# Optimization experiments

Hardware: AMD Instinct MI355X
Metric: run time of the kernel (lower is better)

Reference implementation:

```python
import jax, jax.numpy as jnp
import numpy as np

def setup_inputs() -> dict:
    key = jax.random.key(0)
    k1, k2 = jax.random.split(key)
    B, S, D, R = 16, 1024, 1024, 128
    batch = jax.random.normal(k1, (B, S, D), dtype=jnp.float32)
    # probe parameter initialized uniform(-0.05, 0.05) as in the torch module
    proj = jax.random.uniform(k2, (D, R), dtype=jnp.float32, minval=-0.05, maxval=0.05)
    return {"batch": batch, "proj": proj}

def reference(batch, proj):
    # transformed: [B, S, R]
    t = jnp.matmul(batch, proj)
    # squared L2 distances for all pairs: ||t_i||^2 + ||t_j||^2 - 2 t_i . t_j
    sq_norms = jnp.sum(t * t, axis=-1)                      # [B, S]
    cross = jnp.einsum('bir,bjr->bij', t, t)                # [B, S, S]
    d = sq_norms[:, :, None] + sq_norms[:, None, :] - 2.0 * cross
    return jnp.maximum(d, 0.0)  # clamp tiny negative values from the identity
```

## Files before the change

kernel.cpp:

```cpp
#include <hip/hip_runtime.h>

typedef __attribute__((ext_vector_type(8))) __bf16 bf16x8;
typedef __attribute__((ext_vector_type(4))) float f32x4;
typedef const __attribute__((address_space(1))) unsigned int gu32;
typedef __attribute__((address_space(3))) unsigned int lu32;

#define B_ 16
#define S_ 1024
#define D_ 1024
#define R_ 128

__device__ __forceinline__ void gl16(const void* g, void* l) {
    __builtin_amdgcn_global_load_lds((gu32*)g, (lu32*)l, 16, 0, 0);
}

__global__ __launch_bounds__(256) void k_transpose(const float* __restrict__ proj,
                                                   __bf16* __restrict__ projT) {
    __shared__ __bf16 tile[64][66];
    const int k0 = blockIdx.x * 64;
    const int r0 = blockIdx.y * 64;
#pragma unroll
    for (int it = 0; it < 16; ++it) {
        int idx = it * 256 + threadIdx.x;
        int kk = idx >> 6, rr = idx & 63;
        tile[kk][rr] = (__bf16)proj[(size_t)(k0 + kk) * R_ + (r0 + rr)];
    }
    __syncthreads();
#pragma unroll
    for (int it = 0; it < 16; ++it) {
        int idx = it * 256 + threadIdx.x;
        int rr = idx >> 6, kk = idx & 63;
        projT[(size_t)(r0 + rr) * D_ + (k0 + kk)] = tile[kk][rr];
    }
}

__global__ __launch_bounds__(256, 4) void k_proj(const float* __restrict__ batch,
                                                 const __bf16* __restrict__ projT,
                                                 __bf16* __restrict__ t,
                                                 float* __restrict__ sqn) {
    __shared__ __align__(16) char smem[40960];
    const int wave = threadIdx.x >> 6;
    const int lane = threadIdx.x & 63;
    const int ln = lane & 15, q = lane >> 4;
    const int m0 = blockIdx.x * 16;

    const int arow = wave * 4 + (lane >> 4);
    const int aswz = ((arow & 7) << 5) | ((arow & 8) << 1);
    const char* ag = (const char*)batch + (size_t)(m0 + arow) * 4096
                   + (((lane & 15) * 16) ^ aswz);
    const int brx = wave * 8 + (lane >> 3);
    const int bswz = (brx & 7) << 4;
    const char* bg = (const char*)projT + (size_t)brx * 2048
                   + (((lane & 7) * 16) ^ bswz);
    char* const abuf0 = smem + wave * 1024;
    char* const bbuf0 = smem + 8192 + wave * 1024;

    const int raswz = ((ln & 7) << 5) | ((ln & 8) << 1);
    const int rbswz = (ln & 7) << 4;
    const int kq = q * 32;
    const int kq2 = q * 16;

    f32x4 acc[2];
    acc[0] = f32x4{0.f, 0.f, 0.f, 0.f};
    acc[1] = f32x4{0.f, 0.f, 0.f, 0.f};

    gl16(ag, abuf0);
#pragma unroll
    for (int s = 0; s < 4; ++s) gl16(bg + (size_t)s * 65536, bbuf0 + s * 4096);
    __syncthreads();

#pragma unroll 2
    for (int c = 0; c < 16; ++c) {
        const int cur = c & 1, nxt = cur ^ 1;
        if (c < 15) {
            gl16(ag + (c + 1) * 256, abuf0 + nxt * 4096);
#pragma unroll
            for (int s = 0; s < 4; ++s)
                gl16(bg + (size_t)s * 65536 + (c + 1) * 128,
                     bbuf0 + nxt * 16384 + s * 4096);
        }
        const char* ab = smem + cur * 4096 + ln * 256;
        const char* bb = smem + 8192 + cur * 16384 + ln * 128;
#pragma unroll
        for (int ks = 0; ks < 2; ++ks) {
            float4 lo = *(const float4*)(ab + ((ks * 128 + kq) ^ raswz));
            float4 hi = *(const float4*)(ab + ((ks * 128 + kq + 16) ^ raswz));
            bf16x8 af;
            af[0] = (__bf16)lo.x; af[1] = (__bf16)lo.y;
            af[2] = (__bf16)lo.z; af[3] = (__bf16)lo.w;
            af[4] = (__bf16)hi.x; af[5] = (__bf16)hi.y;
            af[6] = (__bf16)hi.z; af[7] = (__bf16)hi.w;
            const int ko = (ks * 64 + kq2) ^ rbswz;
            bf16x8 bf0 = *(const bf16x8*)(bb + (wave * 2 + 0) * 2048 + ko);
            bf16x8 bf1 = *(const bf16x8*)(bb + (wave * 2 + 1) * 2048 + ko);
            acc[0] = __builtin_amdgcn_mfma_f32_16x16x32_bf16(af, bf0, acc[0], 0, 0, 0);
            acc[1] = __builtin_amdgcn_mfma_f32_16x16x32_bf16(af, bf1, acc[1], 0, 0, 0);
        }
        __syncthreads();
    }

    float* sqpart = (float*)smem;
    float sq[4] = {0.f, 0.f, 0.f, 0.f};
#pragma unroll
    for (int p = 0; p < 2; ++p) {
        const int ni = wave * 2 + p;
        f32x4 v = acc[p];
#pragma unroll
        for (int r = 0; r < 4; ++r) {
            __bf16 h = (__bf16)v[r];
            t[(size_t)(m0 + q * 4 + r) * R_ + ni * 16 + ln] = h;
            float f = (float)h;
            sq[r] += f * f;
        }
    }
#pragma unroll
    for (int r = 0; r < 4; ++r) {
#pragma unroll
        for (int off = 1; off < 16; off <<= 1)
            sq[r] += __shfl_xor(sq[r], off, 64);
    }
    if (ln == 0) {
#pragma unroll
        for (int r = 0; r < 4; ++r) sqpart[wave * 16 + q * 4 + r] = sq[r];
    }
    __syncthreads();
    if (threadIdx.x < 16) {
        float s = sqpart[threadIdx.x] + sqpart[16 + threadIdx.x] +
                  sqpart[32 + threadIdx.x] + sqpart[48 + threadIdx.x];
        sqn[m0 + threadIdx.x] = s;
    }
}

__global__ __launch_bounds__(256, 2) void k_gram(const __bf16* __restrict__ t,
                                                 const float* __restrict__ sqn,
                                                 float* __restrict__ out) {
    __shared__ __align__(16) char smem[65536];
    const int b = blockIdx.z;
    const int wave = threadIdx.x >> 6, lane = threadIdx.x & 63;
    const int ln = lane & 15, q = lane >> 4;
    const int wi = wave >> 1, wj = wave & 1;
    const int i0b = blockIdx.y * 128, j0b = blockIdx.x * 128;
    const __bf16* tb = t + (size_t)b * S_ * R_;
    const float* sqb = sqn + (size_t)b * S_;

    const int grow = wave * 4 + (lane >> 4);
    const int gwin = ((lane & 15) * 16) ^ ((grow & 7) << 4);
    const char* agt = (const char*)tb + (size_t)(i0b + grow) * 256 + gwin;
    const char* bgt = (const char*)tb + (size_t)(j0b + grow) * 256 + gwin;
    char* const adst = smem + wave * 1024;
    char* const bdst = smem + 32768 + wave * 1024;
#pragma unroll
    for (int s = 0; s < 8; ++s) gl16(agt + (size_t)s * 4096, adst + s * 4096);
#pragma unroll
    for (int s = 0; s < 8; ++s) gl16(bgt + (size_t)s * 4096, bdst + s * 4096);

    float sqj[4];
#pragma unroll
    for (int ni = 0; ni < 4; ++ni) sqj[ni] = sqb[j0b + wj * 64 + ni * 16 + ln];
    __syncthreads();

    f32x4 acc[4][4];
#pragma unroll
    for (int mi = 0; mi < 4; ++mi)
#pragma unroll
        for (int ni = 0; ni < 4; ++ni) acc[mi][ni] = f32x4{0.f, 0.f, 0.f, 0.f};

    const int rsw = (ln & 7) << 4;
    const char* abA = smem + (size_t)(wi * 64 + ln) * 256;
    const char* abB = smem + 32768 + (size_t)(wj * 64 + ln) * 256;
#pragma unroll
    for (int ks = 0; ks < 4; ++ks) {
        const int ko = (ks * 64 + q * 16) ^ rsw;
        bf16x8 af[4], bfm[4];
#pragma unroll
        for (int mi = 0; mi < 4; ++mi)
            af[mi] = *(const bf16x8*)(abA + mi * 4096 + ko);
#pragma unroll
        for (int ni = 0; ni < 4; ++ni)
            bfm[ni] = *(const bf16x8*)(abB + ni * 4096 + ko);
#pragma unroll
        for (int mi = 0; mi < 4; ++mi)
#pragma unroll
            for (int ni = 0; ni < 4; ++ni)
                acc[mi][ni] = __builtin_amdgcn_mfma_f32_16x16x32_bf16(
                    af[mi], bfm[ni], acc[mi][ni], 0, 0, 0);
    }

    const int i0 = i0b + wi * 64, j0 = j0b + wj * 64;
    float* outb = out + (size_t)b * S_ * S_;
#pragma unroll
    for (int mi = 0; mi < 4; ++mi) {
#pragma unroll
        for (int r = 0; r < 4; ++r) {
            const int i = i0 + mi * 16 + q * 4 + r;
            const float si = sqb[i];
            float* orow = outb + (size_t)i * S_ + j0;
#pragma unroll
            for (int ni = 0; ni < 4; ++ni) {
                float v = si + sqj[ni] - 2.f * acc[mi][ni][r];
                orow[ni * 16 + ln] = fmaxf(v, 0.f);
            }
        }
    }
}

extern "C" void kernel_launch(void* const* d_in, const int* in_sizes, int n_in,
                              void* d_out, int out_size, void* d_ws, size_t ws_size,
                              hipStream_t stream) {
    const float* batch = (const float*)d_in[0];
    const float* proj  = (const float*)d_in[1];
    float* out = (float*)d_out;

    char* ws = (char*)d_ws;
    __bf16* t     = (__bf16*)ws;
    __bf16* projT = (__bf16*)(ws + (size_t)B_ * S_ * R_ * 2);
    float*  sqn   = (float*)(ws + (size_t)B_ * S_ * R_ * 2
                                + (size_t)R_ * D_ * 2);

    k_transpose<<<dim3(D_ / 64, R_ / 64), 256, 0, stream>>>(proj, projT);
    k_proj<<<dim3((B_ * S_) / 16), 256, 0, stream>>>(batch, projT, t, sqn);
    k_gram<<<dim3(S_ / 128, S_ / 128, B_), 256, 0, stream>>>(t, sqn, out);
}
```

Measured before the change: 141.5 us.

## Retile projection kernel and split gram loads into two pipelined halves

The projection kernel moves to 512-thread blocks covering 32 rows with a 2x4 wave grid. Each stage now loads a wider K chunk, and explicit vmcnt waits plus raw barriers replace __syncthreads, so the next chunk's loads overlap compute. The gram kernel splits its K=128 load into two halves so MFMA work on the first half can start while the second is still in flight, and it writes the output with nontemporal stores. The tradeoff is much larger LDS use in the projection kernel (96KB), which lowers occupancy, and the correctness of the hand-written waitcnt counts depends on how the compiler orders the loads.

```diff
diff --git a/kernel.cpp b/kernel.cpp
--- a/kernel.cpp
+++ b/kernel.cpp
@@ -34,81 +34,87 @@
     }
 }
 
-__global__ __launch_bounds__(256, 4) void k_proj(const float* __restrict__ batch,
+__global__ __launch_bounds__(512, 2) void k_proj(const float* __restrict__ batch,
                                                  const __bf16* __restrict__ projT,
                                                  __bf16* __restrict__ t,
                                                  float* __restrict__ sqn) {
-    __shared__ __align__(16) char smem[40960];
-    const int wave = threadIdx.x >> 6;
-    const int lane = threadIdx.x & 63;
+    __shared__ __align__(16) char smem[98304];
+    const int tid = threadIdx.x;
+    const int wave = tid >> 6, lane = tid & 63;
     const int ln = lane & 15, q = lane >> 4;
-    const int m0 = blockIdx.x * 16;
-
-    const int arow = wave * 4 + (lane >> 4);
-    const int aswz = ((arow & 7) << 5) | ((arow & 8) << 1);
-    const char* ag = (const char*)batch + (size_t)(m0 + arow) * 4096
-                   + (((lane & 15) * 16) ^ aswz);
-    const int brx = wave * 8 + (lane >> 3);
-    const int bswz = (brx & 7) << 4;
-    const char* bg = (const char*)projT + (size_t)brx * 2048
-                   + (((lane & 7) * 16) ^ bswz);
-    char* const abuf0 = smem + wave * 1024;
-    char* const bbuf0 = smem + 8192 + wave * 1024;
-
-    const int raswz = ((ln & 7) << 5) | ((ln & 8) << 1);
-    const int rbswz = (ln & 7) << 4;
-    const int kq = q * 32;
-    const int kq2 = q * 16;
+    const int wr = wave >> 2, wc = wave & 3;
+    const int m0 = blockIdx.x * 32;
+
+    const int ar0 = wave * 2 + (lane >> 5);
+    const int aoff = ((lane & 31) * 16) ^ (((ar0 & 7) << 5) | ((ar0 & 8) << 1));
+    const char* ag0 = (const char*)batch + (size_t)(m0 + ar0) * 4096 + aoff;
+    const char* ag1 = ag0 + (size_t)16 * 4096;
+    const int bn0 = wave * 4 + (lane >> 4);
+    const int boff = ((lane & 15) * 16) ^ ((bn0 & 7) << 4);
+    const char* bg = (const char*)projT + (size_t)bn0 * 2048 + boff;
+    char* const adst = smem + wave * 1024;
+    char* const bdst = smem + 32768 + wave * 1024;
+
+    const int aswz = ((ln & 7) << 5) | ((ln & 8) << 1);
+    const int bswz = (ln & 7) << 4;
+    const char* arow_l = smem + (size_t)(wr * 16 + ln) * 512;
+    const char* brow_l = smem + 32768 + (size_t)(wc * 32 + ln) * 256;
 
     f32x4 acc[2];
     acc[0] = f32x4{0.f, 0.f, 0.f, 0.f};
     acc[1] = f32x4{0.f, 0.f, 0.f, 0.f};
 
-    gl16(ag, abuf0);
-#pragma unroll
-    for (int s = 0; s < 4; ++s) gl16(bg + (size_t)s * 65536, bbuf0 + s * 4096);
-    __syncthreads();
-
-#pragma unroll 2
-    for (int c = 0; c < 16; ++c) {
-        const int cur = c & 1, nxt = cur ^ 1;
-        if (c < 15) {
-            gl16(ag + (c + 1) * 256, abuf0 + nxt * 4096);
-#pragma unroll
-            for (int s = 0; s < 4; ++s)
-                gl16(bg + (size_t)s * 65536 + (c + 1) * 128,
-                     bbuf0 + nxt * 16384 + s * 4096);
-        }
-        const char* ab = smem + cur * 4096 + ln * 256;
-        const char* bb = smem + 8192 + cur * 16384 + ln * 128;
-#pragma unroll
-        for (int ks = 0; ks < 2; ++ks) {
-            float4 lo = *(const float4*)(ab + ((ks * 128 + kq) ^ raswz));
-            float4 hi = *(const float4*)(ab + ((ks * 128 + kq + 16) ^ raswz));
+#define STAGE_P(c, buf)                                                     \
+    do {                                                                    \
+        gl16(ag0 + (c) * 512, adst + (buf) * 16384);                        \
+        gl16(ag1 + (c) * 512, adst + (buf) * 16384 + 8192);                 \
+        gl16(bg + (c) * 256,                 bdst + (buf) * 32768);         \
+        gl16(bg + 32 * 2048 + (c) * 256,     bdst + (buf) * 32768 + 8192);  \
+        gl16(bg + 64 * 2048 + (c) * 256,     bdst + (buf) * 32768 + 16384); \
+        gl16(bg + 96 * 2048 + (c) * 256,     bdst + (buf) * 32768 + 24576); \
+    } while (0)
+
+    STAGE_P(0, 0);
+#pragma unroll
+    for (int c = 0; c < 8; ++c) {
+        const int buf = c & 1;
+        if (c < 7) {
+            STAGE_P(c + 1, buf ^ 1);
+            asm volatile("s_waitcnt vmcnt(6)" ::: "memory");
+        } else {
+            asm volatile("s_waitcnt vmcnt(0)" ::: "memory");
+        }
+        __builtin_amdgcn_s_barrier();
+        const char* Ab = arow_l + buf * 16384;
+        const char* Bb = brow_l + buf * 32768;
+#pragma unroll
+        for (int ks = 0; ks < 4; ++ks) {
+            const int ao = ks * 128 + q * 32;
+            float4 lo = *(const float4*)(Ab + (ao ^ aswz));
+            float4 hi = *(const float4*)(Ab + ((ao + 16) ^ aswz));
             bf16x8 af;
             af[0] = (__bf16)lo.x; af[1] = (__bf16)lo.y;
             af[2] = (__bf16)lo.z; af[3] = (__bf16)lo.w;
             af[4] = (__bf16)hi.x; af[5] = (__bf16)hi.y;
             af[6] = (__bf16)hi.z; af[7] = (__bf16)hi.w;
-            const int ko = (ks * 64 + kq2) ^ rbswz;
-            bf16x8 bf0 = *(const bf16x8*)(bb + (wave * 2 + 0) * 2048 + ko);
-            bf16x8 bf1 = *(const bf16x8*)(bb + (wave * 2 + 1) * 2048 + ko);
-            acc[0] = __builtin_amdgcn_mfma_f32_16x16x32_bf16(af, bf0, acc[0], 0, 0, 0);
-            acc[1] = __builtin_amdgcn_mfma_f32_16x16x32_bf16(af, bf1, acc[1], 0, 0, 0);
-        }
-        __syncthreads();
-    }
+            const int bo = (ks * 64 + q * 16) ^ bswz;
+            bf16x8 b0 = *(const bf16x8*)(Bb + bo);
+            bf16x8 b1 = *(const bf16x8*)(Bb + 4096 + bo);
+            acc[0] = __builtin_amdgcn_mfma_f32_16x16x32_bf16(af, b0, acc[0], 0, 0, 0);
+            acc[1] = __builtin_amdgcn_mfma_f32_16x16x32_bf16(af, b1, acc[1], 0, 0, 0);
+        }
+        __builtin_amdgcn_s_barrier();
+    }
+#undef STAGE_P
 
     float* sqpart = (float*)smem;
     float sq[4] = {0.f, 0.f, 0.f, 0.f};
 #pragma unroll
     for (int p = 0; p < 2; ++p) {
-        const int ni = wave * 2 + p;
-        f32x4 v = acc[p];
 #pragma unroll
         for (int r = 0; r < 4; ++r) {
-            __bf16 h = (__bf16)v[r];
-            t[(size_t)(m0 + q * 4 + r) * R_ + ni * 16 + ln] = h;
+            __bf16 h = (__bf16)acc[p][r];
+            t[(size_t)(m0 + wr * 16 + q * 4 + r) * R_ + wc * 32 + p * 16 + ln] = h;
             float f = (float)h;
             sq[r] += f * f;
         }
@@ -121,13 +127,13 @@
     }
     if (ln == 0) {
 #pragma unroll
-        for (int r = 0; r < 4; ++r) sqpart[wave * 16 + q * 4 + r] = sq[r];
+        for (int r = 0; r < 4; ++r)
+            sqpart[wc * 32 + wr * 16 + q * 4 + r] = sq[r];
     }
     __syncthreads();
-    if (threadIdx.x < 16) {
-        float s = sqpart[threadIdx.x] + sqpart[16 + threadIdx.x] +
-                  sqpart[32 + threadIdx.x] + sqpart[48 + threadIdx.x];
-        sqn[m0 + threadIdx.x] = s;
+    if (tid < 32) {
+        float s = sqpart[tid] + sqpart[32 + tid] + sqpart[64 + tid] + sqpart[96 + tid];
+        sqn[m0 + tid] = s;
     }
 }
 
@@ -143,21 +149,32 @@
     const __bf16* tb = t + (size_t)b * S_ * R_;
     const float* sqb = sqn + (size_t)b * S_;
 
-    const int grow = wave * 4 + (lane >> 4);
-    const int gwin = ((lane & 15) * 16) ^ ((grow & 7) << 4);
-    const char* agt = (const char*)tb + (size_t)(i0b + grow) * 256 + gwin;
-    const char* bgt = (const char*)tb + (size_t)(j0b + grow) * 256 + gwin;
+    float sqj[4];
+#pragma unroll
+    for (int ni = 0; ni < 4; ++ni) sqj[ni] = sqb[j0b + wj * 64 + ni * 16 + ln];
+
+    const int grow = wave * 8 + (lane >> 3);
+    const int goff = ((lane & 7) * 16) ^ ((grow & 7) << 4);
+    const char* agt = (const char*)tb + (size_t)(i0b + grow) * 256 + goff;
+    const char* bgt = (const char*)tb + (size_t)(j0b + grow) * 256 + goff;
     char* const adst = smem + wave * 1024;
-    char* const bdst = smem + 32768 + wave * 1024;
-#pragma unroll
-    for (int s = 0; s < 8; ++s) gl16(agt + (size_t)s * 4096, adst + s * 4096);
-#pragma unroll
-    for (int s = 0; s < 8; ++s) gl16(bgt + (size_t)s * 4096, bdst + s * 4096);
-
-    float sqj[4];
-#pragma unroll
-    for (int ni = 0; ni < 4; ++ni) sqj[ni] = sqb[j0b + wj * 64 + ni * 16 + ln];
-    __syncthreads();
+    char* const bdst = smem + 16384 + wave * 1024;
+
+#define STAGE_G(h)                                                        \
+    do {                                                                  \
+        gl16(agt + (h) * 128,              adst + (h) * 32768);           \
+        gl16(agt + 32 * 256 + (h) * 128,   adst + (h) * 32768 + 4096);    \
+        gl16(agt + 64 * 256 + (h) * 128,   adst + (h) * 32768 + 8192);    \
+        gl16(agt + 96 * 256 + (h) * 128,   adst + (h) * 32768 + 12288);   \
+        gl16(bgt + (h) * 128,              bdst + (h) * 32768);           \
+        gl16(bgt + 32 * 256 + (h) * 128,   bdst + (h) * 32768 + 4096);    \
+        gl16(bgt + 64 * 256 + (h) * 128,   bdst + (h) * 32768 + 8192);    \
+        gl16(bgt + 96 * 256 + (h) * 128,   bdst + (h) * 32768 + 12288);   \
+    } while (0)
+
+    STAGE_G(0);
+    STAGE_G(1);
+#undef STAGE_G
 
     f32x4 acc[4][4];
 #pragma unroll
@@ -166,24 +183,35 @@
         for (int ni = 0; ni < 4; ++ni) acc[mi][ni] = f32x4{0.f, 0.f, 0.f, 0.f};
 
     const int rsw = (ln & 7) << 4;
-    const char* abA = smem + (size_t)(wi * 64 + ln) * 256;
-    const char* abB = smem + 32768 + (size_t)(wj * 64 + ln) * 256;
-#pragma unroll
-    for (int ks = 0; ks < 4; ++ks) {
-        const int ko = (ks * 64 + q * 16) ^ rsw;
-        bf16x8 af[4], bfm[4];
-#pragma unroll
-        for (int mi = 0; mi < 4; ++mi)
-            af[mi] = *(const bf16x8*)(abA + mi * 4096 + ko);
-#pragma unroll
-        for (int ni = 0; ni < 4; ++ni)
-            bfm[ni] = *(const bf16x8*)(abB + ni * 4096 + ko);
-#pragma unroll
-        for (int mi = 0; mi < 4; ++mi)
+    const char* abA = smem + (size_t)(wi * 64 + ln) * 128;
+    const char* abB = smem + 16384 + (size_t)(wj * 64 + ln) * 128;
+
+#pragma unroll
+    for (int h = 0; h < 2; ++h) {
+        if (h == 0)
+            asm volatile("s_waitcnt vmcnt(8)" ::: "memory");
+        else
+            asm volatile("s_waitcnt vmcnt(0)" ::: "memory");
+        __builtin_amdgcn_s_barrier();
+        const char* hA = abA + h * 32768;
+        const char* hB = abB + h * 32768;
+#pragma unroll
+        for (int ks = 0; ks < 2; ++ks) {
+            const int ko = (ks * 64 + q * 16) ^ rsw;
+            bf16x8 af[4], bfm[4];
+#pragma unroll
+            for (int mi = 0; mi < 4; ++mi)
+                af[mi] = *(const bf16x8*)(hA + mi * 2048 + ko);
 #pragma unroll
             for (int ni = 0; ni < 4; ++ni)
-                acc[mi][ni] = __builtin_amdgcn_mfma_f32_16x16x32_bf16(
-                    af[mi], bfm[ni], acc[mi][ni], 0, 0, 0);
+                bfm[ni] = *(const bf16x8*)(hB + ni * 2048 + ko);
+#pragma unroll
+            for (int mi = 0; mi < 4; ++mi)
+#pragma unroll
+                for (int ni = 0; ni < 4; ++ni)
+                    acc[mi][ni] = __builtin_amdgcn_mfma_f32_16x16x32_bf16(
+                        af[mi], bfm[ni], acc[mi][ni], 0, 0, 0);
+        }
     }
 
     const int i0 = i0b + wi * 64, j0 = j0b + wj * 64;
@@ -198,7 +226,7 @@
 #pragma unroll
             for (int ni = 0; ni < 4; ++ni) {
                 float v = si + sqj[ni] - 2.f * acc[mi][ni][r];
-                orow[ni * 16 + ln] = fmaxf(v, 0.f);
+                __builtin_nontemporal_store(fmaxf(v, 0.f), &orow[ni * 16 + ln]);
             }
         }
     }
@@ -218,6 +246,6 @@
                                 + (size_t)R_ * D_ * 2);
 
     k_transpose<<<dim3(D_ / 64, R_ / 64), 256, 0, stream>>>(proj, projT);
-    k_proj<<<dim3((B_ * S_) / 16), 256, 0, stream>>>(batch, projT, t, sqn);
+    k_proj<<<dim3((B_ * S_) / 32), 512, 0, stream>>>(batch, projT, t, sqn);
     k_gram<<<dim3(S_ / 128, S_ / 128, B_), 256, 0, stream>>>(t, sqn, out);
 }
```

New measurement: 141.2 us. About the same (-0.3%).

## Use fine-grained vmcnt waits and split-K staging in projection and gram kernels

Applied to the files above, without the earlier changes.

The projection kernel's K loop is fully unrolled and replaces __syncthreads with explicit s_waitcnt vmcnt counts plus raw barriers, so the next stage's async LDS loads stay in flight while the current stage computes. The gram kernel splits its K=128 load into two halves with a new LDS layout, so MFMA work on the first half can start while the second half is still arriving. Output stores become nontemporal to avoid polluting cache with the large streaming result. The manual vmcnt counts depend on the exact number of outstanding loads, which is fragile if the compiler reorders or adds memory ops.

```diff
diff --git a/kernel.cpp b/kernel.cpp
--- a/kernel.cpp
+++ b/kernel.cpp
@@ -64,23 +64,28 @@
     acc[0] = f32x4{0.f, 0.f, 0.f, 0.f};
     acc[1] = f32x4{0.f, 0.f, 0.f, 0.f};
 
-    gl16(ag, abuf0);
-#pragma unroll
-    for (int s = 0; s < 4; ++s) gl16(bg + (size_t)s * 65536, bbuf0 + s * 4096);
-    __syncthreads();
-
-#pragma unroll 2
+#define STAGE_P(c, buf)                                                      \
+    do {                                                                     \
+        gl16(ag + (c) * 256, abuf0 + (buf) * 4096);                          \
+        gl16(bg + (c) * 128,                 bbuf0 + (buf) * 16384);         \
+        gl16(bg + 32 * 2048 + (c) * 128,     bbuf0 + (buf) * 16384 + 4096);  \
+        gl16(bg + 64 * 2048 + (c) * 128,     bbuf0 + (buf) * 16384 + 8192);  \
+        gl16(bg + 96 * 2048 + (c) * 128,     bbuf0 + (buf) * 16384 + 12288); \
+    } while (0)
+
+    STAGE_P(0, 0);
+#pragma unroll
     for (int c = 0; c < 16; ++c) {
-        const int cur = c & 1, nxt = cur ^ 1;
+        const int buf = c & 1;
         if (c < 15) {
-            gl16(ag + (c + 1) * 256, abuf0 + nxt * 4096);
-#pragma unroll
-            for (int s = 0; s < 4; ++s)
-                gl16(bg + (size_t)s * 65536 + (c + 1) * 128,
-                     bbuf0 + nxt * 16384 + s * 4096);
-        }
-        const char* ab = smem + cur * 4096 + ln * 256;
-        const char* bb = smem + 8192 + cur * 16384 + ln * 128;
+            STAGE_P(c + 1, buf ^ 1);
+            asm volatile("s_waitcnt vmcnt(5)" ::: "memory");
+        } else {
+            asm volatile("s_waitcnt vmcnt(0)" ::: "memory");
+        }
+        __builtin_amdgcn_s_barrier();
+        const char* ab = smem + buf * 4096 + ln * 256;
+        const char* bb = smem + 8192 + buf * 16384 + ln * 128;
 #pragma unroll
         for (int ks = 0; ks < 2; ++ks) {
             float4 lo = *(const float4*)(ab + ((ks * 128 + kq) ^ raswz));
@@ -96,8 +101,9 @@
             acc[0] = __builtin_amdgcn_mfma_f32_16x16x32_bf16(af, bf0, acc[0], 0, 0, 0);
             acc[1] = __builtin_amdgcn_mfma_f32_16x16x32_bf16(af, bf1, acc[1], 0, 0, 0);
         }
-        __syncthreads();
-    }
+        __builtin_amdgcn_s_barrier();
+    }
+#undef STAGE_P
 
     float* sqpart = (float*)smem;
     float sq[4] = {0.f, 0.f, 0.f, 0.f};
@@ -143,21 +149,32 @@
     const __bf16* tb = t + (size_t)b * S_ * R_;
     const float* sqb = sqn + (size_t)b * S_;
 
-    const int grow = wave * 4 + (lane >> 4);
-    const int gwin = ((lane & 15) * 16) ^ ((grow & 7) << 4);
-    const char* agt = (const char*)tb + (size_t)(i0b + grow) * 256 + gwin;
-    const char* bgt = (const char*)tb + (size_t)(j0b + grow) * 256 + gwin;
+    float sqj[4];
+#pragma unroll
+    for (int ni = 0; ni < 4; ++ni) sqj[ni] = sqb[j0b + wj * 64 + ni * 16 + ln];
+
+    const int grow = wave * 8 + (lane >> 3);
+    const int goff = ((lane & 7) * 16) ^ ((grow & 7) << 4);
+    const char* agt = (const char*)tb + (size_t)(i0b + grow) * 256 + goff;
+    const char* bgt = (const char*)tb + (size_t)(j0b + grow) * 256 + goff;
     char* const adst = smem + wave * 1024;
-    char* const bdst = smem + 32768 + wave * 1024;
-#pragma unroll
-    for (int s = 0; s < 8; ++s) gl16(agt + (size_t)s * 4096, adst + s * 4096);
-#pragma unroll
-    for (int s = 0; s < 8; ++s) gl16(bgt + (size_t)s * 4096, bdst + s * 4096);
-
-    float sqj[4];
-#pragma unroll
-    for (int ni = 0; ni < 4; ++ni) sqj[ni] = sqb[j0b + wj * 64 + ni * 16 + ln];
-    __syncthreads();
+    char* const bdst = smem + 16384 + wave * 1024;
+
+#define STAGE_G(h)                                                        \
+    do {                                                                  \
+        gl16(agt + (h) * 128,              adst + (h) * 32768);           \
+        gl16(agt + 32 * 256 + (h) * 128,   adst + (h) * 32768 + 4096);    \
+        gl16(agt + 64 * 256 + (h) * 128,   adst + (h) * 32768 + 8192);    \
+        gl16(agt + 96 * 256 + (h) * 128,   adst + (h) * 32768 + 12288);   \
+        gl16(bgt + (h) * 128,              bdst + (h) * 32768);           \
+        gl16(bgt + 32 * 256 + (h) * 128,   bdst + (h) * 32768 + 4096);    \
+        gl16(bgt + 64 * 256 + (h) * 128,   bdst + (h) * 32768 + 8192);    \
+        gl16(bgt + 96 * 256 + (h) * 128,   bdst + (h) * 32768 + 12288);   \
+    } while (0)
+
+    STAGE_G(0);
+    STAGE_G(1);
+#undef STAGE_G
 
     f32x4 acc[4][4];
 #pragma unroll
@@ -166,24 +183,35 @@
         for (int ni = 0; ni < 4; ++ni) acc[mi][ni] = f32x4{0.f, 0.f, 0.f, 0.f};
 
     const int rsw = (ln & 7) << 4;
-    const char* abA = smem + (size_t)(wi * 64 + ln) * 256;
-    const char* abB = smem + 32768 + (size_t)(wj * 64 + ln) * 256;
-#pragma unroll
-    for (int ks = 0; ks < 4; ++ks) {
-        const int ko = (ks * 64 + q * 16) ^ rsw;
-        bf16x8 af[4], bfm[4];
-#pragma unroll
-        for (int mi = 0; mi < 4; ++mi)
-            af[mi] = *(const bf16x8*)(abA + mi * 4096 + ko);
-#pragma unroll
-        for (int ni = 0; ni < 4; ++ni)
-            bfm[ni] = *(const bf16x8*)(abB + ni * 4096 + ko);
-#pragma unroll
-        for (int mi = 0; mi < 4; ++mi)
+    const char* abA = smem + (size_t)(wi * 64 + ln) * 128;
+    const char* abB = smem + 16384 + (size_t)(wj * 64 + ln) * 128;
+
+#pragma unroll
+    for (int h = 0; h < 2; ++h) {
+        if (h == 0)
+            asm volatile("s_waitcnt vmcnt(8)" ::: "memory");
+        else
+            asm volatile("s_waitcnt vmcnt(0)" ::: "memory");
+        __builtin_amdgcn_s_barrier();
+        const char* hA = abA + h * 32768;
+        const char* hB = abB + h * 32768;
+#pragma unroll
+        for (int ks = 0; ks < 2; ++ks) {
+            const int ko = (ks * 64 + q * 16) ^ rsw;
+            bf16x8 af[4], bfm[4];
+#pragma unroll
+            for (int mi = 0; mi < 4; ++mi)
+                af[mi] = *(const bf16x8*)(hA + mi * 2048 + ko);
 #pragma unroll
             for (int ni = 0; ni < 4; ++ni)
-                acc[mi][ni] = __builtin_amdgcn_mfma_f32_16x16x32_bf16(
-                    af[mi], bfm[ni], acc[mi][ni], 0, 0, 0);
+                bfm[ni] = *(const bf16x8*)(hB + ni * 2048 + ko);
+#pragma unroll
+            for (int mi = 0; mi < 4; ++mi)
+#pragma unroll
+                for (int ni = 0; ni < 4; ++ni)
+                    acc[mi][ni] = __builtin_amdgcn_mfma_f32_16x16x32_bf16(
+                        af[mi], bfm[ni], acc[mi][ni], 0, 0, 0);
+        }
     }
 
     const int i0 = i0b + wi * 64, j0 = j0b + wj * 64;
@@ -198,7 +226,7 @@
 #pragma unroll
             for (int ni = 0; ni < 4; ++ni) {
                 float v = si + sqj[ni] - 2.f * acc[mi][ni][r];
-                orow[ni * 16 + ln] = fmaxf(v, 0.f);
+                __builtin_nontemporal_store(fmaxf(v, 0.f), &orow[ni * 16 + ln]);
             }
         }
     }
```

Result: no change. 139.4 us (median of 2 runs) (-1.5%).
